# Kernel tuning notes

Hardware: AMD Instinct MI355X
Metric: run time of the kernel (lower is better)

## Reference

```python
import jax, jax.numpy as jnp
import numpy as np
import math

B, S, D, H, W = 4, 8192, 1024, 16, 512  # batch, seq, d_model, heads, attention_window
HD = D // H


def setup_inputs() -> dict:
    key = jax.random.key(0)
    ks = jax.random.split(key, 5)
    scale = 0.02
    return {
        "x": jax.random.normal(ks[0], (B, S, D), dtype=jnp.float32),
        "wq": jax.random.normal(ks[1], (D, D), dtype=jnp.float32) * scale,
        "bq": jnp.zeros((D,), dtype=jnp.float32),
        "wk": jax.random.normal(ks[2], (D, D), dtype=jnp.float32) * scale,
        "bk": jnp.zeros((D,), dtype=jnp.float32),
        "wv": jax.random.normal(ks[3], (D, D), dtype=jnp.float32) * scale,
        "bv": jnp.zeros((D,), dtype=jnp.float32),
        "wo": jax.random.normal(ks[4], (D, D), dtype=jnp.float32) * scale,
        "bo": jnp.zeros((D,), dtype=jnp.float32),
    }


def reference(x, wq, bq, wk, bk, wv, bv, wo, bo):
    # torch Linear: y = x @ W.T + b
    q = (x @ wq.T + bq).reshape(B, S, H, HD)
    k = (x @ wk.T + bk).reshape(B, S, H, HD)
    v = (x @ wv.T + bv).reshape(B, S, H, HD)

    nb = S // W  # number of query blocks
    qb = q.reshape(B, nb, W, H, HD)

    # pad keys/values by W at the front so every block sees a 2W key window
    kp = jnp.pad(k, ((0, 0), (W, 0), (0, 0), (0, 0)))
    vp = jnp.pad(v, ((0, 0), (W, 0), (0, 0), (0, 0)))
    # padded key indices for block n: [n*W, n*W + 2W) <-> original [n*W - W, n*W + W)
    idx = jnp.arange(nb)[:, None] * W + jnp.arange(2 * W)[None, :]  # [nb, 2W]
    kb = kp[:, idx]  # [B, nb, 2W, H, HD]
    vb = vp[:, idx]  # [B, nb, 2W, H, HD]

    scores = jnp.einsum('bnqhd,bnkhd->bnhqk', qb, kb) / math.sqrt(HD)
    valid = (idx >= W)  # padded (out-of-range) keys only occur for block 0
    scores = jnp.where(valid[None, :, None, None, :], scores, -jnp.inf)
    attn = jax.nn.softmax(scores, axis=-1)  # softmax over the block's key window

    out = jnp.einsum('bnhqk,bnkhd->bnqhd', attn, vb).reshape(B, S, D)
    return out @ wo.T + bo
```

## Files before the change

### kernel.cpp

```cpp
#include <hip/hip_runtime.h>
#include <hip/hip_bf16.h>
#include <cstdint>

typedef __bf16 bf16;
typedef __attribute__((ext_vector_type(8))) __bf16 bf16x8;
typedef __attribute__((ext_vector_type(4))) __bf16 bf16x4;
typedef __attribute__((ext_vector_type(4))) float f32x4;
typedef __attribute__((ext_vector_type(16))) float f32x16;
typedef __attribute__((ext_vector_type(4))) unsigned int u32x4;

#define B_ 4
#define S_ 8192
#define D_ 1024
#define H_ 16
#define HD_ 64
#define W_ 512
#define M_ (B_*S_)

#define EXP2F(x) __builtin_amdgcn_exp2f(x)
#define MFMA16(a,b,c) __builtin_amdgcn_mfma_f32_16x16x32_bf16(a,b,c,0,0,0)
#define MFMA32(a,b,c) __builtin_amdgcn_mfma_f32_32x32x16_bf16(a,b,c,0,0,0)

__device__ __forceinline__ void async16(const void* g, void* l) {
  __builtin_amdgcn_global_load_lds(
      (const __attribute__((address_space(1))) unsigned int*)g,
      (__attribute__((address_space(3))) unsigned int*)l, 16, 0, 0);
}

__device__ __forceinline__ void cast_region(const float* __restrict__ in,
                                            bf16* __restrict__ out, int n4,
                                            int i0, int stride) {
  for (int i = i0; i < n4; i += stride) {
    f32x4 v = ((const f32x4*)in)[i];
    bf16x4 o = { (bf16)v[0], (bf16)v[1], (bf16)v[2], (bf16)v[3] };
    ((bf16x4*)out)[i] = o;
  }
}

__global__ void cast_all(const float* __restrict__ x,  bf16* __restrict__ xb,
                         const float* __restrict__ wq, bf16* __restrict__ wqb,
                         const float* __restrict__ wk, bf16* __restrict__ wkb,
                         const float* __restrict__ wv, bf16* __restrict__ wvb,
                         const float* __restrict__ wo, bf16* __restrict__ wob) {
  int i0 = blockIdx.x * blockDim.x + threadIdx.x;
  int stride = gridDim.x * blockDim.x;
  cast_region(x,  xb,  M_*D_/4, i0, stride);
  cast_region(wq, wqb, D_*D_/4, i0, stride);
  cast_region(wk, wkb, D_*D_/4, i0, stride);
  cast_region(wv, wvb, D_*D_/4, i0, stride);
  cast_region(wo, wob, D_*D_/4, i0, stride);
}

#define GEMM_BODY(Ab_, Bb_)                                                     \
  f32x4 acc[8][4] = {};                                                         \
  const int srow16 = tid & 15;                                                  \
  const int skb    = ((tid >> 4) & 3) * 16;                                     \
  auto stageA = [&](int t2) {                                                   \
    _Pragma("unroll")                                                           \
    for (int j = 0; j < 2; ++j) {                                               \
      int f = j * 8 + (tid >> 6);                                               \
      char* dst = lds + (t2 & 3) * 32768 + j * 8192 + tid * 16;                 \
      async16(Ab_ + (size_t)(f * 16 + srow16) * (K * 2) + t2 * 64 + skb, dst);  \
    }                                                                           \
  };                                                                            \
  auto stageB = [&](int t2) {                                                   \
    _Pragma("unroll")                                                           \
    for (int j = 0; j < 2; ++j) {                                               \
      int f = j * 8 + (tid >> 6);                                               \
      char* dst = lds + (t2 & 3) * 32768 + 16384 + j * 8192 + tid * 16;         \
      async16(Bb_ + (size_t)(f * 16 + srow16) * (K * 2) + t2 * 64 + skb, dst);  \
    }                                                                           \
  };                                                                            \
  auto compute = [&](int sl, int qm) {                                          \
    const char* ab = lds + sl * 32768;                                          \
    const char* bb = ab + 16384;                                                \
    bf16x8 a[4], b[4];                                                          \
    _Pragma("unroll")                                                           \
    for (int r = 0; r < 4; ++r)                                                 \
      a[r] = *(const bf16x8*)(ab + (wr * 8 + qm * 4 + r) * 1024 + lane * 16);   \
    _Pragma("unroll")                                                           \
    for (int c = 0; c < 4; ++c)                                                 \
      b[c] = *(const bf16x8*)(bb + (wc * 4 + c) * 1024 + lane * 16);            \
    asm volatile("s_waitcnt lgkmcnt(0)" ::: "memory");                          \
    __builtin_amdgcn_sched_barrier(0);                                          \
    __builtin_amdgcn_s_setprio(1);                                              \
    _Pragma("unroll")                                                           \
    for (int r = 0; r < 4; ++r)                                                 \
      _Pragma("unroll")                                                         \
      for (int c = 0; c < 4; ++c)                                               \
        acc[qm * 4 + r][c] = MFMA16(a[r], b[c], acc[qm * 4 + r][c]);            \
    __builtin_amdgcn_s_setprio(0);                                              \
  };                                                                            \
  stageA(0); stageB(0); stageA(1); stageB(1);                                   \
  _Pragma("unroll 1")                                                           \
  for (int it = 0; it < 16; ++it) {                                             \
    int e = 2 * it;                                                             \
    bool full = (it < 15);                                                      \
    if (full) { stageA(e + 2);                                                  \
      asm volatile("s_waitcnt vmcnt(6)" ::: "memory");                          \
    } else {                                                                    \
      asm volatile("s_waitcnt vmcnt(4)" ::: "memory");                          \
    }                                                                           \
    __builtin_amdgcn_s_barrier();                                               \
    compute(e & 3, 0);                                                          \
    __builtin_amdgcn_s_barrier();                                               \
    if (full) stageB(e + 2);                                                    \
    __builtin_amdgcn_s_barrier();                                               \
    compute(e & 3, 1);                                                          \
    __builtin_amdgcn_s_barrier();                                               \
    if (full) { stageA(e + 3);                                                  \
      asm volatile("s_waitcnt vmcnt(6)" ::: "memory");                          \
    } else {                                                                    \
      asm volatile("s_waitcnt vmcnt(0)" ::: "memory");                          \
    }                                                                           \
    __builtin_amdgcn_s_barrier();                                               \
    compute((e + 1) & 3, 0);                                                    \
    __builtin_amdgcn_s_barrier();                                               \
    if (full) stageB(e + 3);                                                    \
    __builtin_amdgcn_s_barrier();                                               \
    compute((e + 1) & 3, 1);                                                    \
    __builtin_amdgcn_s_barrier();                                               \
  }

__global__ void __launch_bounds__(512, 2) gemm_qkv3(
    const bf16* __restrict__ A,
    const bf16* __restrict__ Wq, const bf16* __restrict__ Wk, const bf16* __restrict__ Wv,
    const float* __restrict__ Bq, const float* __restrict__ Bk, const float* __restrict__ Bv,
    bf16* __restrict__ Oq, bf16* __restrict__ Ok, bf16* __restrict__ Ovt, float qscale)
{
  constexpr int K = D_, N = D_;
  __shared__ char lds[4 * 32768];
  int bid = blockIdx.x;
  int seg = bid >> 9;
  int sbid = bid & 511;
  int nid = (sbid & 7) * 64 + (sbid >> 3);
  int bm = nid >> 2, bn = nid & 3;
  const bf16* Bw = (seg == 0) ? Wq : (seg == 1) ? Wk : Wv;
  const float* bias = (seg == 0) ? Bq : (seg == 1) ? Bk : Bv;
  float scale = (seg == 0) ? qscale : 1.0f;
  const int tid = threadIdx.x, lane = tid & 63;
  const int w = tid >> 6, wr = w >> 2, wc = w & 3;
  const char* Ab = (const char*)(A + (size_t)bm * 256 * K);
  const char* Bb = (const char*)(Bw + (size_t)bn * 256 * K);

  GEMM_BODY(Ab, Bb)

  int row0 = bm * 256 + wr * 128, col0 = bn * 256 + wc * 64;
  int rsub = (lane >> 4) * 4;
  if (seg < 2) {
    bf16* outp = (seg == 0) ? Oq : Ok;
#pragma unroll
    for (int cb = 0; cb < 4; ++cb) {
      int col = col0 + cb * 16 + (lane & 15);
      float bz = bias[col];
#pragma unroll
      for (int rb = 0; rb < 8; ++rb)
#pragma unroll
        for (int reg = 0; reg < 4; ++reg) {
          int row = row0 + rb * 16 + rsub + reg;
          outp[(size_t)row * N + col] = (bf16)((acc[rb][cb][reg] + bz) * scale);
        }
    }
  } else {
#pragma unroll
    for (int cb = 0; cb < 4; ++cb) {
      int col = col0 + cb * 16 + (lane & 15);
      float bz = bias[col];
#pragma unroll
      for (int rb = 0; rb < 8; ++rb) {
        int row = row0 + rb * 16 + rsub;
        bf16x4 ov;
#pragma unroll
        for (int reg = 0; reg < 4; ++reg)
          ov[reg] = (bf16)(acc[rb][cb][reg] + bz);
        *(bf16x4*)&Ovt[((size_t)(row >> 13) * D_ + col) * S_ + (row & (S_-1))] = ov;
      }
    }
  }
}

__global__ void __launch_bounds__(512, 2) gemm_out(
    const bf16* __restrict__ A, const bf16* __restrict__ Bw,
    const float* __restrict__ bias, float* __restrict__ outp)
{
  constexpr int K = D_, N = D_;
  __shared__ char lds[4 * 32768];
  int bid = blockIdx.x;
  int nid = (bid & 7) * 64 + (bid >> 3);
  int bm = nid >> 2, bn = nid & 3;
  const int tid = threadIdx.x, lane = tid & 63;
  const int w = tid >> 6, wr = w >> 2, wc = w & 3;
  const char* Ab = (const char*)(A + (size_t)bm * 256 * K);
  const char* Bb = (const char*)(Bw + (size_t)bn * 256 * K);

  GEMM_BODY(Ab, Bb)

  int row0 = bm * 256 + wr * 128, col0 = bn * 256 + wc * 64;
  int rsub = (lane >> 4) * 4;
#pragma unroll
  for (int cb = 0; cb < 4; ++cb) {
    int col = col0 + cb * 16 + (lane & 15);
    float bz = bias[col];
#pragma unroll
    for (int rb = 0; rb < 8; ++rb)
#pragma unroll
      for (int reg = 0; reg < 4; ++reg) {
        int row = row0 + rb * 16 + rsub + reg;
        outp[(size_t)row * N + col] = acc[rb][cb][reg] + bz;
      }
  }
}

__global__ void __launch_bounds__(256, 4) attn_kernel(
    const bf16* __restrict__ Q, const bf16* __restrict__ Kb,
    const bf16* __restrict__ Vt, bf16* __restrict__ Ao)
{
  __shared__ char Klds[2][8192];
  __shared__ char Vlds[2][8192];
  int x = blockIdx.x;
  int qt = (x >> 3) & 3;
  int g  = (x & 7) + 8 * (x >> 5);
  int h = g & 15, n = (g >> 4) & 15, b = g >> 8;
  int tid = threadIdx.x, lane = tid & 63, w = tid >> 6;
  int hi = lane >> 5, qv = lane & 31;
  int qrow = n * W_ + qt * 128 + w * 32;

  const bf16* Qrow = Q + ((size_t)(b * S_ + qrow + qv)) * D_ + h * 64;
  bf16x8 Qf[4];
#pragma unroll
  for (int s = 0; s < 4; ++s) Qf[s] = *(const bf16x8*)(Qrow + s * 16 + hi * 8);

  const bf16* Kg = Kb + ((size_t)b * S_) * D_ + h * 64;
  const bf16* Vg = Vt + ((size_t)(b * H_ + h) * HD_) * S_;

  const int srow = tid >> 3;
  const int sseg = (tid & 7) ^ (srow & 7);
  const int fswq = (qv & 7) << 4;

  f32x16 O0 = {}, O1 = {};
  float l_r = 0.f;

  const int c0 = (n == 0) ? 8 : 0;
  const int ksbase = (n - 1) * W_;

  auto stage = [&](int c) {
    int ks = ksbase + c * 64;
    int so = (c & 1) * 8192;
    const bf16* kr = Kg + (size_t)(ks + srow) * D_ + sseg * 8;
    async16(kr,                    &Klds[0][0] + so + tid * 16);
    async16(kr + 32 * D_,          &Klds[0][0] + so + 4096 + tid * 16);
    const bf16* vr = Vg + (size_t)srow * S_ + ks + sseg * 8;
    async16(vr,                    &Vlds[0][0] + so + tid * 16);
    async16(vr + (size_t)32 * S_,  &Vlds[0][0] + so + 4096 + tid * 16);
  };

  stage(c0);
  asm volatile("s_waitcnt vmcnt(0)" ::: "memory");
  __builtin_amdgcn_s_barrier();

#pragma unroll 1
  for (int c = c0; c < 16; ++c) {
    if (c + 1 < 16) stage(c + 1);
    const char* kbuf = &Klds[0][0] + (c & 1) * 8192;
    const char* vbuf = &Vlds[0][0] + (c & 1) * 8192;
    f32x16 C0 = {}, C1 = {};
    __builtin_amdgcn_s_setprio(1);
#pragma unroll
    for (int s = 0; s < 4; ++s) {
      bf16x8 k0 = *(const bf16x8*)(kbuf + qv * 128        + ((s * 32 + hi * 16) ^ fswq));
      bf16x8 k1 = *(const bf16x8*)(kbuf + (32 + qv) * 128 + ((s * 32 + hi * 16) ^ fswq));
      C0 = MFMA32(k0, Qf[s], C0);
      C1 = MFMA32(k1, Qf[s], C1);
    }
    __builtin_amdgcn_s_setprio(0);
    float p0[16], p1[16];
#pragma unroll
    for (int r = 0; r < 16; ++r) {
      p0[r] = EXP2F(C0[r]);
      p1[r] = EXP2F(C1[r]);
    }
    float q0[8];
#pragma unroll
    for (int i = 0; i < 8; ++i)
      q0[i] = (p0[2*i] + p0[2*i+1]) + (p1[2*i] + p1[2*i+1]);
    l_r += ((q0[0] + q0[1]) + (q0[2] + q0[3])) + ((q0[4] + q0[5]) + (q0[6] + q0[7]));
    unsigned int L0[8], L1[8];
#pragma unroll
    for (int t = 0; t < 8; ++t) {
      asm("v_cvt_pk_bf16_f32 %0, %1, %2" : "=v"(L0[t]) : "v"(p0[2*t]), "v"(p0[2*t+1]));
      asm("v_cvt_pk_bf16_f32 %0, %1, %2" : "=v"(L1[t]) : "v"(p1[2*t]), "v"(p1[2*t+1]));
    }
    asm volatile("v_permlane32_swap_b32 %0, %1" : "+v"(L0[0]), "+v"(L0[2]));
    asm volatile("v_permlane32_swap_b32 %0, %1" : "+v"(L0[1]), "+v"(L0[3]));
    asm volatile("v_permlane32_swap_b32 %0, %1" : "+v"(L0[4]), "+v"(L0[6]));
    asm volatile("v_permlane32_swap_b32 %0, %1" : "+v"(L0[5]), "+v"(L0[7]));
    asm volatile("v_permlane32_swap_b32 %0, %1" : "+v"(L1[0]), "+v"(L1[2]));
    asm volatile("v_permlane32_swap_b32 %0, %1" : "+v"(L1[1]), "+v"(L1[3]));
    asm volatile("v_permlane32_swap_b32 %0, %1" : "+v"(L1[4]), "+v"(L1[6]));
    asm volatile("v_permlane32_swap_b32 %0, %1" : "+v"(L1[5]), "+v"(L1[7]));
    u32x4 F[2][2];
    F[0][0] = u32x4{L0[0], L0[1], L0[2], L0[3]};
    F[0][1] = u32x4{L0[4], L0[5], L0[6], L0[7]};
    F[1][0] = u32x4{L1[0], L1[1], L1[2], L1[3]};
    F[1][1] = u32x4{L1[4], L1[5], L1[6], L1[7]};
    __builtin_amdgcn_s_setprio(1);
#pragma unroll
    for (int T = 0; T < 2; ++T)
#pragma unroll
      for (int s = 0; s < 2; ++s) {
        bf16x8 pf = *(bf16x8*)&F[T][s];
        int kbyteoff = T * 64 + s * 32 + hi * 16;
        bf16x8 v0 = *(const bf16x8*)(vbuf + qv * 128        + (kbyteoff ^ fswq));
        bf16x8 v1 = *(const bf16x8*)(vbuf + (32 + qv) * 128 + (kbyteoff ^ fswq));
        O0 = MFMA32(v0, pf, O0);
        O1 = MFMA32(v1, pf, O1);
      }
    __builtin_amdgcn_s_setprio(0);
    asm volatile("s_waitcnt vmcnt(0)" ::: "memory");
    __builtin_amdgcn_s_barrier();
  }
  float lt = l_r + __shfl_xor(l_r, 32);
  float inv = 1.0f / lt;
  size_t obase = ((size_t)(b * S_ + qrow + qv)) * D_ + h * 64;
#pragma unroll
  for (int ot = 0; ot < 2; ++ot) {
#pragma unroll
    for (int rq = 0; rq < 4; ++rq) {
      int hd = ot * 32 + 8 * rq + 4 * hi;
      bf16x4 ov;
#pragma unroll
      for (int j = 0; j < 4; ++j) {
        float val = (ot == 0 ? O0[rq*4 + j] : O1[rq*4 + j]) * inv;
        ov[j] = (bf16)val;
      }
      *(bf16x4*)(Ao + obase + hd) = ov;
    }
  }
}

extern "C" void kernel_launch(void* const* d_in, const int* in_sizes, int n_in,
                              void* d_out, int out_size, void* d_ws, size_t ws_size,
                              hipStream_t stream) {
  const float* x  = (const float*)d_in[0];
  const float* wq = (const float*)d_in[1];
  const float* bq = (const float*)d_in[2];
  const float* wk = (const float*)d_in[3];
  const float* bk = (const float*)d_in[4];
  const float* wv = (const float*)d_in[5];
  const float* bv = (const float*)d_in[6];
  const float* wo = (const float*)d_in[7];
  const float* bo = (const float*)d_in[8];
  float* out = (float*)d_out;

  char* ws = (char*)d_ws;
  const size_t sz = (size_t)M_ * D_ * 2;
  bf16* xb  = (bf16*)(ws + 0*sz);
  bf16* qb  = (bf16*)(ws + 1*sz);
  bf16* kb  = (bf16*)(ws + 2*sz);
  bf16* vt  = (bf16*)(ws + 3*sz);
  bf16* ao  = (bf16*)(ws + 4*sz);
  bf16* wqb = (bf16*)(ws + 5*sz);
  bf16* wkb = wqb + (size_t)D_*D_;
  bf16* wvb = wkb + (size_t)D_*D_;
  bf16* wob = wvb + (size_t)D_*D_;

  cast_all<<<2048, 256, 0, stream>>>(x, xb, wq, wqb, wk, wkb, wv, wvb, wo, wob);

  gemm_qkv3<<<1536, 512, 0, stream>>>(xb, wqb, wkb, wvb, bq, bk, bv,
                                      qb, kb, vt, 0.125f * 1.44269504f);

  attn_kernel<<<4096, 256, 0, stream>>>(qb, kb, vt, ao);

  gemm_out<<<512, 512, 0, stream>>>(ao, wob, bo, out);
}
```

Measured before the change: 536.2 us.

## Restructure GEMM main loop with register double-buffered fragments and deeper prefetch

Rewrites the shared GEMM body so that A and B tiles are staged together three steps ahead. LDS fragments for the next k-step are loaded into a second register set while MFMAs run on the current one, replacing the split half-tile compute with several barriers per step. Launch bounds drop to one block per CU so the extra fragment registers fit, which lowers occupancy. The aim is to hide LDS read latency and cut barrier overhead in the QKV and output projections.

```diff
diff --git a/kernel.cpp b/kernel.cpp
--- a/kernel.cpp
+++ b/kernel.cpp
@@ -55,74 +55,76 @@
   f32x4 acc[8][4] = {};                                                         \
   const int srow16 = tid & 15;                                                  \
   const int skb    = ((tid >> 4) & 3) * 16;                                     \
-  auto stageA = [&](int t2) {                                                   \
+  auto stageT = [&](int t2) {                                                   \
     _Pragma("unroll")                                                           \
     for (int j = 0; j < 2; ++j) {                                               \
       int f = j * 8 + (tid >> 6);                                               \
-      char* dst = lds + (t2 & 3) * 32768 + j * 8192 + tid * 16;                 \
-      async16(Ab_ + (size_t)(f * 16 + srow16) * (K * 2) + t2 * 64 + skb, dst);  \
+      async16(Ab_ + (size_t)(f * 16 + srow16) * (K * 2) + t2 * 64 + skb,        \
+              lds + (t2 & 3) * 32768 + j * 8192 + tid * 16);                    \
+    }                                                                           \
+    _Pragma("unroll")                                                           \
+    for (int j = 0; j < 2; ++j) {                                               \
+      int f = j * 8 + (tid >> 6);                                               \
+      async16(Bb_ + (size_t)(f * 16 + srow16) * (K * 2) + t2 * 64 + skb,        \
+              lds + (t2 & 3) * 32768 + 16384 + j * 8192 + tid * 16);            \
     }                                                                           \
   };                                                                            \
-  auto stageB = [&](int t2) {                                                   \
-    _Pragma("unroll")                                                           \
-    for (int j = 0; j < 2; ++j) {                                               \
-      int f = j * 8 + (tid >> 6);                                               \
-      char* dst = lds + (t2 & 3) * 32768 + 16384 + j * 8192 + tid * 16;         \
-      async16(Bb_ + (size_t)(f * 16 + srow16) * (K * 2) + t2 * 64 + skb, dst);  \
-    }                                                                           \
-  };                                                                            \
-  auto compute = [&](int sl, int qm) {                                          \
-    const char* ab = lds + sl * 32768;                                          \
+  auto ldfrag = [&](int t2, bf16x8 (&a)[8], bf16x8 (&b)[4]) {                   \
+    const char* ab = lds + (t2 & 3) * 32768;                                    \
     const char* bb = ab + 16384;                                                \
-    bf16x8 a[4], b[4];                                                          \
-    _Pragma("unroll")                                                           \
-    for (int r = 0; r < 4; ++r)                                                 \
-      a[r] = *(const bf16x8*)(ab + (wr * 8 + qm * 4 + r) * 1024 + lane * 16);   \
+    _Pragma("unroll")                                                           \
+    for (int r = 0; r < 8; ++r)                                                 \
+      a[r] = *(const bf16x8*)(ab + (wr * 8 + r) * 1024 + lane * 16);            \
     _Pragma("unroll")                                                           \
     for (int c = 0; c < 4; ++c)                                                 \
       b[c] = *(const bf16x8*)(bb + (wc * 4 + c) * 1024 + lane * 16);            \
+  };                                                                            \
+  auto mma = [&](bf16x8 (&a)[8], bf16x8 (&b)[4]) {                              \
+    __builtin_amdgcn_s_setprio(1);                                              \
+    _Pragma("unroll")                                                           \
+    for (int r = 0; r < 8; ++r)                                                 \
+      _Pragma("unroll")                                                         \
+      for (int c = 0; c < 4; ++c)                                               \
+        acc[r][c] = MFMA16(a[r], b[c], acc[r][c]);                              \
+    __builtin_amdgcn_s_setprio(0);                                              \
+  };                                                                            \
+  bf16x8 aC[8], bC[4], aN[8], bN[4];                                            \
+  stageT(0); stageT(1); stageT(2);                                              \
+  asm volatile("s_waitcnt vmcnt(8)" ::: "memory");                              \
+  __builtin_amdgcn_s_barrier();                                                 \
+  __builtin_amdgcn_sched_barrier(0);                                            \
+  ldfrag(0, aC, bC);                                                            \
+  _Pragma("unroll 1")                                                           \
+  for (int it = 0; it < 16; ++it) {                                             \
+    int t = 2 * it;                                                             \
+             \
+    if (t <= 28) { stageT(t + 3);                                               \
+      asm volatile("s_waitcnt vmcnt(8)" ::: "memory");                          \
+    } else {                                        \
+      asm volatile("s_waitcnt vmcnt(0)" ::: "memory");                          \
+    }                                                                           \
     asm volatile("s_waitcnt lgkmcnt(0)" ::: "memory");                          \
     __builtin_amdgcn_sched_barrier(0);                                          \
-    __builtin_amdgcn_s_setprio(1);                                              \
-    _Pragma("unroll")                                                           \
-    for (int r = 0; r < 4; ++r)                                                 \
-      _Pragma("unroll")                                                         \
-      for (int c = 0; c < 4; ++c)                                               \
-        acc[qm * 4 + r][c] = MFMA16(a[r], b[c], acc[qm * 4 + r][c]);            \
-    __builtin_amdgcn_s_setprio(0);                                              \
-  };                                                                            \
-  stageA(0); stageB(0); stageA(1); stageB(1);                                   \
-  _Pragma("unroll 1")                                                           \
-  for (int it = 0; it < 16; ++it) {                                             \
-    int e = 2 * it;                                                             \
-    bool full = (it < 15);                                                      \
-    if (full) { stageA(e + 2);                                                  \
-      asm volatile("s_waitcnt vmcnt(6)" ::: "memory");                          \
-    } else {                                                                    \
+    __builtin_amdgcn_s_barrier();                                               \
+    __builtin_amdgcn_sched_barrier(0);                                          \
+    mma(aC, bC);                                                                \
+    ldfrag(t + 1, aN, bN);                                                      \
+        \
+    int u = t + 1;                                                              \
+    if (u <= 28) { stageT(u + 3);                                               \
+      asm volatile("s_waitcnt vmcnt(8)" ::: "memory");                          \
+    } else if (u == 29) {                                                       \
       asm volatile("s_waitcnt vmcnt(4)" ::: "memory");                          \
-    }                                                                           \
+    }                                         \
+    asm volatile("s_waitcnt lgkmcnt(0)" ::: "memory");                          \
+    __builtin_amdgcn_sched_barrier(0);                                          \
     __builtin_amdgcn_s_barrier();                                               \
-    compute(e & 3, 0);                                                          \
-    __builtin_amdgcn_s_barrier();                                               \
-    if (full) stageB(e + 2);                                                    \
-    __builtin_amdgcn_s_barrier();                                               \
-    compute(e & 3, 1);                                                          \
-    __builtin_amdgcn_s_barrier();                                               \
-    if (full) { stageA(e + 3);                                                  \
-      asm volatile("s_waitcnt vmcnt(6)" ::: "memory");                          \
-    } else {                                                                    \
-      asm volatile("s_waitcnt vmcnt(0)" ::: "memory");                          \
-    }                                                                           \
-    __builtin_amdgcn_s_barrier();                                               \
-    compute((e + 1) & 3, 0);                                                    \
-    __builtin_amdgcn_s_barrier();                                               \
-    if (full) stageB(e + 3);                                                    \
-    __builtin_amdgcn_s_barrier();                                               \
-    compute((e + 1) & 3, 1);                                                    \
-    __builtin_amdgcn_s_barrier();                                               \
-  }
-
-__global__ void __launch_bounds__(512, 2) gemm_qkv3(
+    __builtin_amdgcn_sched_barrier(0);                                          \
+    mma(aN, bN);                                                                \
+    if (u < 31) ldfrag(u + 1, aC, bC);                                          \
+  }
+
+__global__ void __launch_bounds__(512, 1) gemm_qkv3(
     const bf16* __restrict__ A,
     const bf16* __restrict__ Wq, const bf16* __restrict__ Wk, const bf16* __restrict__ Wv,
     const float* __restrict__ Bq, const float* __restrict__ Bk, const float* __restrict__ Bv,
@@ -179,7 +181,7 @@
   }
 }
 
-__global__ void __launch_bounds__(512, 2) gemm_out(
+__global__ void __launch_bounds__(512, 1) gemm_out(
     const bf16* __restrict__ A, const bf16* __restrict__ Bw,
     const float* __restrict__ bias, float* __restrict__ outp)
 {
```

After: 537.2 us. Within noise of the previous version (+0.2%).
